# Performance work log

Measured on AMD Instinct MI355X. Metric: run time of the kernel, lower is better.

## Reference

```python
import jax, jax.numpy as jnp
import numpy as np

PRE_HEIGHT = 96
PRE_WIDTH = 128


def setup_inputs() -> dict:
    key = jax.random.key(0)
    B, K, H, W = 32, 64, 96, 128
    x = jax.random.normal(key, (B, K, H, W), dtype=jnp.float32)
    return {"combined_hm_preds": x, "batch_size": B, "num_of_kp": K}


def reference(combined_hm_preds, batch_size, num_of_kp):
    B, K, H, W = combined_hm_preds.shape
    # nn.Softmax() with no dim on a 4D tensor -> softmax over dim=1 (channels)
    map_val_all = jax.nn.softmax(combined_hm_preds, axis=1)
    # zeta[b,k] = sum over spatial of the channel-softmaxed map
    get_zeta = map_val_all.sum(axis=(2, 3))  # [B, K]
    js = jnp.arange(W, dtype=map_val_all.dtype)
    iis = jnp.arange(H, dtype=map_val_all.dtype)
    # per-channel weighted coordinate sums
    Sx = jnp.einsum('bkij,j->bk', map_val_all, js)  # [B, K]
    Sy = jnp.einsum('bkij,i->bk', map_val_all, iis)  # [B, K]
    # faithful to the original: accumulators are never reset across k or b,
    # so each keypoint uses the inclusive cumulative sum in flattened (b,k) order
    cum_x = jnp.cumsum(Sx.reshape(-1)).reshape(B, K)
    cum_y = jnp.cumsum(Sy.reshape(-1)).reshape(B, K)
    kx = jnp.round(cum_x / get_zeta)
    ky = jnp.round(cum_y / get_zeta)
    # out-of-range clamp to the image center, as in the original
    kx = jnp.where((kx > PRE_WIDTH) | (kx < 0), PRE_WIDTH * 0.5, kx)
    ky = jnp.where((ky > PRE_HEIGHT) | (ky < 0), PRE_HEIGHT * 0.5, ky)
    keypoint = jnp.stack([kx, ky], axis=-1)  # [B, K, 2]
    return (map_val_all, keypoint, get_zeta)
```

## Files before the change

### kernel.cpp

```cpp
#include <hip/hip_runtime.h>
#include <math.h>

#define BB 32
#define KK 64
#define HH 96
#define WW 128
#define HW (HH*WW)
#define MAP_SIZE (BB*KK*HW)
#define NBK (BB*KK)
#define NT  (HW/256)

__global__ __launch_bounds__(256, 4) void fused_k(const float* __restrict__ x,
                                                  float* __restrict__ out,
                                                  double* __restrict__ sxyz) {
    int blk  = blockIdx.x;
    int b    = blk / NT;
    int tile = blk - b * NT;
    int t    = threadIdx.x;
    size_t base = (size_t)b * (KK * HW) + (size_t)tile * 256 + t;

    float e[KK];
    float den = 0.f;
    #pragma unroll
    for (int k = 0; k < KK; ++k) {
        e[k] = __expf(__builtin_nontemporal_load(&x[base + (size_t)k * HW]));
        den += e[k];
    }
    float inv = 1.f / den;

    #pragma unroll
    for (int k = 0; k < KK; ++k) {
        out[base + (size_t)k * HW] = e[k] * inv;
    }

    __syncthreads();

    int k = t >> 2;
    int q = t & 3;
    const float* mp = out + (size_t)b * (KK * HW) + (size_t)k * HW + tile * 256;
    const double gy_base = (double)(tile * 2);
    double z = 0.0, sx = 0.0, sy = 0.0;
    #pragma unroll
    for (int j = 0; j < 16; ++j) {
        int p = q * 4 + j * 16;
        float4 v = *reinterpret_cast<const float4*>(mp + p);
        double m0 = (double)v.x, m1 = (double)v.y, m2 = (double)v.z, m3 = (double)v.w;
        double s = ((m0 + m1) + m2) + m3;
        double gx0 = (double)(p & (WW - 1));
        z  += s;
        sx += s * gx0 + (m1 + 2.0 * m2 + 3.0 * m3);
        sy += s * (gy_base + (double)(p >> 7));
    }

    z  += __shfl_xor(z,  1, 64);  z  += __shfl_xor(z,  2, 64);
    sx += __shfl_xor(sx, 1, 64);  sx += __shfl_xor(sx, 2, 64);
    sy += __shfl_xor(sy, 1, 64);  sy += __shfl_xor(sy, 2, 64);
    if (q == 0) {
        int bk = b * KK + k;
        atomicAdd(&sxyz[bk * 3 + 0], sx);
        atomicAdd(&sxyz[bk * 3 + 1], sy);
        atomicAdd(&sxyz[bk * 3 + 2], z);
    }
}

__global__ __launch_bounds__(256) void keypoint_k(const double* __restrict__ sxyz,
                                                  float* __restrict__ kp,
                                                  float* __restrict__ zeta) {
    const int PT = NBK / 256;
    int t = threadIdx.x;
    int lane = t & 63, wid = t >> 6;

    double vx[PT], vy[PT], vz[PT];
    double cx = 0.0, cy = 0.0;
    #pragma unroll
    for (int e = 0; e < PT; ++e) {
        int idx = t * PT + e;
        cx += sxyz[idx * 3 + 0]; vx[e] = cx;
        cy += sxyz[idx * 3 + 1]; vy[e] = cy;
        vz[e] = sxyz[idx * 3 + 2];
    }
    double tx = cx, ty = cy;
    for (int off = 1; off < 64; off <<= 1) {
        double ax = __shfl_up(tx, off, 64);
        double ay = __shfl_up(ty, off, 64);
        if (lane >= off) { tx += ax; ty += ay; }
    }
    __shared__ double wxs[4], wys[4];
    if (lane == 63) { wxs[wid] = tx; wys[wid] = ty; }
    __syncthreads();
    double offx = tx - cx, offy = ty - cy;
    for (int w2 = 0; w2 < wid; ++w2) { offx += wxs[w2]; offy += wys[w2]; }

    #pragma unroll
    for (int e = 0; e < PT; ++e) {
        int idx = t * PT + e;
        double zz = vz[e];
        double kx = rint((vx[e] + offx) / zz);
        double ky = rint((vy[e] + offy) / zz);
        float fkx = (float)kx, fky = (float)ky;
        if (fkx > 128.0f || fkx < 0.0f) fkx = 64.0f;
        if (fky > 96.0f  || fky < 0.0f) fky = 48.0f;
        kp[idx * 2 + 0] = fkx;
        kp[idx * 2 + 1] = fky;
        zeta[idx] = (float)zz;
    }
}

extern "C" void kernel_launch(void* const* d_in, const int* in_sizes, int n_in,
                              void* d_out, int out_size, void* d_ws, size_t ws_size,
                              hipStream_t stream) {
    const float* x = (const float*)d_in[0];
    float* out  = (float*)d_out;
    float* map  = out;
    float* kp   = out + MAP_SIZE;
    float* zeta = out + MAP_SIZE + NBK * 2;
    double* sxyz = (double*)d_ws;

    hipMemsetAsync(d_ws, 0, (size_t)NBK * 3 * sizeof(double), stream);
    fused_k   <<< BB * NT, 256, 0, stream >>> (x, map, sxyz);
    keypoint_k<<< 1,       256, 0, stream >>> (sxyz, kp, zeta);
}
```

Measured before the change: 188.1 us.

## Stage softmax outputs through shared memory for the coordinate reductions

The kernel no longer re-reads the just-written softmax map from global memory for the zeta/Sx/Sy reductions. It writes each 16-channel chunk to an LDS tile and reduces from there, and the global output stores become nontemporal. In exchange it adds eight block barriers per block. The shuffle reduction now only combines lanes within a wave, so fp64 atomics to the workspace rise fourfold.

```diff
diff --git a/kernel.cpp b/kernel.cpp
--- a/kernel.cpp
+++ b/kernel.cpp
@@ -13,6 +13,8 @@
 __global__ __launch_bounds__(256, 4) void fused_k(const float* __restrict__ x,
                                                   float* __restrict__ out,
                                                   double* __restrict__ sxyz) {
+    __shared__ float sm[16][257];
+
     int blk  = blockIdx.x;
     int b    = blk / NT;
     int tile = blk - b * NT;
@@ -28,38 +30,43 @@
     }
     float inv = 1.f / den;
 
+    int i = t & 15;
+    int g = t >> 4;
+    const double dgxb = (double)((g * 16) & (WW - 1));
+    const double dgy  = (double)(tile * 2 + (g >> 3));
+    int bk_base = b * KK;
+
     #pragma unroll
-    for (int k = 0; k < KK; ++k) {
-        out[base + (size_t)k * HW] = e[k] * inv;
-    }
+    for (int c = 0; c < 4; ++c) {
+        #pragma unroll
+        for (int ki = 0; ki < 16; ++ki) {
+            int k = c * 16 + ki;
+            float m = e[k] * inv;
+            __builtin_nontemporal_store(m, &out[base + (size_t)k * HW]);
+            sm[ki][t] = m;
+        }
+        __syncthreads();
 
-    __syncthreads();
+        double z = 0.0, w = 0.0;
+        #pragma unroll
+        for (int j = 0; j < 16; ++j) {
+            double m = (double)sm[i][g * 16 + j];
+            z += m;
+            w += m * (double)j;
+        }
+        double sx = dgxb * z + w;
+        double sy = dgy * z;
 
-    int k = t >> 2;
-    int q = t & 3;
-    const float* mp = out + (size_t)b * (KK * HW) + (size_t)k * HW + tile * 256;
-    const double gy_base = (double)(tile * 2);
-    double z = 0.0, sx = 0.0, sy = 0.0;
-    #pragma unroll
-    for (int j = 0; j < 16; ++j) {
-        int p = q * 4 + j * 16;
-        float4 v = *reinterpret_cast<const float4*>(mp + p);
-        double m0 = (double)v.x, m1 = (double)v.y, m2 = (double)v.z, m3 = (double)v.w;
-        double s = ((m0 + m1) + m2) + m3;
-        double gx0 = (double)(p & (WW - 1));
-        z  += s;
-        sx += s * gx0 + (m1 + 2.0 * m2 + 3.0 * m3);
-        sy += s * (gy_base + (double)(p >> 7));
-    }
-
-    z  += __shfl_xor(z,  1, 64);  z  += __shfl_xor(z,  2, 64);
-    sx += __shfl_xor(sx, 1, 64);  sx += __shfl_xor(sx, 2, 64);
-    sy += __shfl_xor(sy, 1, 64);  sy += __shfl_xor(sy, 2, 64);
-    if (q == 0) {
-        int bk = b * KK + k;
-        atomicAdd(&sxyz[bk * 3 + 0], sx);
-        atomicAdd(&sxyz[bk * 3 + 1], sy);
-        atomicAdd(&sxyz[bk * 3 + 2], z);
+        z  += __shfl_xor(z,  16, 64);  z  += __shfl_xor(z,  32, 64);
+        sx += __shfl_xor(sx, 16, 64);  sx += __shfl_xor(sx, 32, 64);
+        sy += __shfl_xor(sy, 16, 64);  sy += __shfl_xor(sy, 32, 64);
+        if ((t & 63) < 16) {
+            int bk = bk_base + c * 16 + i;
+            atomicAdd(&sxyz[bk * 3 + 0], sx);
+            atomicAdd(&sxyz[bk * 3 + 1], sy);
+            atomicAdd(&sxyz[bk * 3 + 2], z);
+        }
+        __syncthreads();
     }
 }
 
```

Result: slower. 209.7 us (+11.4%).

## Stage exponentials in shared memory and fuse reductions with vectorized map store

Applied to the files above, without the earlier changes.

Each wave now loads 16 channels with float4 nontemporal loads, writes the exponentials to LDS, computes per-pixel denominators from LDS, then normalizes and stores float4 output while reducing zeta and coordinate sums from registers. This drops the second pass that re-read the just-written softmax map from global memory, and the block index is swizzled across batches. In exchange it uses about 66 KB of LDS per block, lowers the occupancy hint to 2, and moves from a 4-lane to a full 64-lane shuffle reduction per channel, adding more shuffles.

```diff
diff --git a/kernel.cpp b/kernel.cpp
--- a/kernel.cpp
+++ b/kernel.cpp
@@ -8,58 +8,78 @@
 #define HW (HH*WW)
 #define MAP_SIZE (BB*KK*HW)
 #define NBK (BB*KK)
-#define NT  (HW/256)
+#define TPX 256
+#define NT (HW/TPX)
+#define NBLK (BB*NT)
+#define STRIDE 260
 
-__global__ __launch_bounds__(256, 4) void fused_k(const float* __restrict__ x,
+typedef float f32x4 __attribute__((ext_vector_type(4)));
+
+__global__ __launch_bounds__(256, 2) void fused_k(const float* __restrict__ x,
                                                   float* __restrict__ out,
                                                   double* __restrict__ sxyz) {
-    int blk  = blockIdx.x;
-    int b    = blk / NT;
-    int tile = blk - b * NT;
-    int t    = threadIdx.x;
-    size_t base = (size_t)b * (KK * HW) + (size_t)tile * 256 + t;
+    __shared__ float sme[KK][STRIDE];
+    __shared__ float sinv[TPX];
 
-    float e[KK];
+    int blk = blockIdx.x;
+    int tau = (blk & 7) * (NBLK / 8) + (blk >> 3);
+    int b    = tau / NT;
+    int tile = tau - b * NT;
+    int t = threadIdx.x;
+    int w = t >> 6;
+    int l = t & 63;
+
+    const size_t planeq = HW / 4;
+    size_t base4 = ((size_t)b * (KK * HW) + (size_t)tile * TPX) / 4 + l;
+    const f32x4* xp = reinterpret_cast<const f32x4*>(x);
+    f32x4*       op = reinterpret_cast<f32x4*>(out);
+
+    #pragma unroll
+    for (int j = 0; j < 16; ++j) {
+        int k = w * 16 + j;
+        f32x4 v = __builtin_nontemporal_load(xp + base4 + (size_t)k * planeq);
+        f32x4 e;
+        e.x = __expf(v.x); e.y = __expf(v.y);
+        e.z = __expf(v.z); e.w = __expf(v.w);
+        *reinterpret_cast<f32x4*>(&sme[k][4 * l]) = e;
+    }
+    __syncthreads();
+
     float den = 0.f;
     #pragma unroll
-    for (int k = 0; k < KK; ++k) {
-        e[k] = __expf(__builtin_nontemporal_load(&x[base + (size_t)k * HW]));
-        den += e[k];
-    }
-    float inv = 1.f / den;
-
-    #pragma unroll
-    for (int k = 0; k < KK; ++k) {
-        out[base + (size_t)k * HW] = e[k] * inv;
-    }
-
+    for (int k = 0; k < KK; ++k) den += sme[k][t];
+    sinv[t] = 1.f / den;
     __syncthreads();
 
-    int k = t >> 2;
-    int q = t & 3;
-    const float* mp = out + (size_t)b * (KK * HW) + (size_t)k * HW + tile * 256;
-    const double gy_base = (double)(tile * 2);
-    double z = 0.0, sx = 0.0, sy = 0.0;
+    f32x4 inv = reinterpret_cast<const f32x4*>(sinv)[l];
+    const int p0 = 4 * l;
+    const double dgx = (double)(p0 & (WW - 1));
+    const double dgy = (double)(tile * (TPX / WW) + (p0 >> 7));
     #pragma unroll
     for (int j = 0; j < 16; ++j) {
-        int p = q * 4 + j * 16;
-        float4 v = *reinterpret_cast<const float4*>(mp + p);
-        double m0 = (double)v.x, m1 = (double)v.y, m2 = (double)v.z, m3 = (double)v.w;
-        double s = ((m0 + m1) + m2) + m3;
-        double gx0 = (double)(p & (WW - 1));
-        z  += s;
-        sx += s * gx0 + (m1 + 2.0 * m2 + 3.0 * m3);
-        sy += s * (gy_base + (double)(p >> 7));
-    }
+        int k = w * 16 + j;
+        f32x4 e = *reinterpret_cast<const f32x4*>(&sme[k][4 * l]);
+        f32x4 m;
+        m.x = e.x * inv.x; m.y = e.y * inv.y;
+        m.z = e.z * inv.z; m.w = e.w * inv.w;
+        op[base4 + (size_t)k * planeq] = m;
 
-    z  += __shfl_xor(z,  1, 64);  z  += __shfl_xor(z,  2, 64);
-    sx += __shfl_xor(sx, 1, 64);  sx += __shfl_xor(sx, 2, 64);
-    sy += __shfl_xor(sy, 1, 64);  sy += __shfl_xor(sy, 2, 64);
-    if (q == 0) {
-        int bk = b * KK + k;
-        atomicAdd(&sxyz[bk * 3 + 0], sx);
-        atomicAdd(&sxyz[bk * 3 + 1], sy);
-        atomicAdd(&sxyz[bk * 3 + 2], z);
+        double m1 = (double)m.y, m2 = (double)m.z, m3 = (double)m.w;
+        double z  = (((double)m.x + m1) + m2) + m3;
+        double sx = dgx * z + (m1 + 2.0 * m2 + 3.0 * m3);
+        double sy = dgy * z;
+        #pragma unroll
+        for (int off = 1; off < 64; off <<= 1) {
+            z  += __shfl_xor(z,  off, 64);
+            sx += __shfl_xor(sx, off, 64);
+            sy += __shfl_xor(sy, off, 64);
+        }
+        if (l == 0) {
+            int bk = b * KK + k;
+            atomicAdd(&sxyz[bk * 3 + 0], sx);
+            atomicAdd(&sxyz[bk * 3 + 1], sy);
+            atomicAdd(&sxyz[bk * 3 + 2], z);
+        }
     }
 }
 
@@ -117,6 +137,6 @@
     double* sxyz = (double*)d_ws;
 
     hipMemsetAsync(d_ws, 0, (size_t)NBK * 3 * sizeof(double), stream);
-    fused_k   <<< BB * NT, 256, 0, stream >>> (x, map, sxyz);
-    keypoint_k<<< 1,       256, 0, stream >>> (sxyz, kp, zeta);
+    fused_k   <<< NBLK, 256, 0, stream >>> (x, map, sxyz);
+    keypoint_k<<< 1,    256, 0, stream >>> (sxyz, kp, zeta);
 }
```

Result: slower. 201.7 us (+7.2%).
